# Optimization experiments

Hardware: AMD Instinct MI355X
Metric: run time of the kernel (lower is better)

The kernel has to match this reference:

```python
import jax, jax.numpy as jnp
import numpy as np

N_NODES = 100000
N_EDGES = 1600000
IN_C, HID_C, OUT_C = 256, 128, 256


def setup_inputs() -> dict:
    key = jax.random.key(0)
    ks = jax.random.split(key, 8)
    x = jax.random.normal(ks[0], (N_NODES, IN_C), dtype=jnp.float32)
    src = jax.random.randint(ks[1], (N_EDGES,), 0, N_NODES, dtype=jnp.int64)
    dst = jnp.sort(jax.random.randint(ks[2], (N_EDGES,), 0, N_NODES, dtype=jnp.int64))
    # GraphConv weight [in, hid] (glorot), bias [hid]
    W_conv = jax.random.normal(ks[3], (IN_C, HID_C), dtype=jnp.float32) * (2.0 / (IN_C + HID_C)) ** 0.5
    b_conv = jnp.zeros((HID_C,), dtype=jnp.float32)
    # torch Linear weights are [out, in]
    W1 = jax.random.normal(ks[4], (HID_C, HID_C), dtype=jnp.float32) * (2.0 / (2 * HID_C)) ** 0.5
    b1 = jax.random.uniform(ks[5], (HID_C,), dtype=jnp.float32, minval=-1.0, maxval=1.0) / np.sqrt(HID_C)
    W2 = jax.random.normal(ks[6], (OUT_C, HID_C), dtype=jnp.float32) * (2.0 / (HID_C + OUT_C)) ** 0.5
    b2 = jax.random.uniform(ks[7], (OUT_C,), dtype=jnp.float32, minval=-1.0, maxval=1.0) / np.sqrt(OUT_C)
    return {"x": x, "src": src, "dst": dst, "W_conv": W_conv, "b_conv": b_conv,
            "W1": W1, "b1": b1, "W2": W2, "b2": b2}


def reference(x, src, dst, W_conv, b_conv, W1, b1, W2, b2):
    N = x.shape[0]
    ones = jnp.ones(src.shape[0], dtype=x.dtype)
    out_deg = jnp.clip(jax.ops.segment_sum(ones, src, num_segments=N), 1.0)  # [N]
    in_deg = jnp.clip(jax.ops.segment_sum(ones, dst, num_segments=N), 1.0)   # [N]
    # DGL GraphConv, norm='both', in_feats > out_feats -> weight applied before aggregation
    h = x * jax.lax.rsqrt(out_deg)[:, None]          # src-side normalization
    h = h @ W_conv                                    # [N, hid]
    m = jax.ops.segment_sum(h[src], dst, num_segments=N, indices_are_sorted=True)
    h = m * jax.lax.rsqrt(in_deg)[:, None] + b_conv   # dst-side normalization + bias
    h = jax.nn.relu(h)
    h = jax.nn.relu(h @ W1.T + b1)
    return h @ W2.T + b2
```

## Files before the change

### kernel.cpp

```cpp
#include <hip/hip_runtime.h>
#include <hip/hip_bf16.h>


typedef __attribute__((ext_vector_type(8))) short short8;
typedef __attribute__((ext_vector_type(4))) float f32x4;

static __device__ __forceinline__ float bf2f(unsigned int u16) {
    union { unsigned int i; float f; } c; c.i = u16 << 16; return c.f;
}
static __device__ __forceinline__ ushort f2bf(float f) {
    union { float f; unsigned int i; } c; c.f = f;
    unsigned int i = c.i;
    return (ushort)((i + 0x7FFFu + ((i >> 16) & 1u)) >> 16);
}

constexpr int NCHUNK   = 256;
constexpr int NBUK_MAX = 512;

__global__ __launch_bounds__(256) void hist1_kernel(
    const int* __restrict__ src, int* __restrict__ M, int nE, int nBuk, int chunkSz)
{
    __shared__ int cnt[NBUK_MAX];
    int c = blockIdx.x, tid = threadIdx.x;
    for (int i = tid; i < nBuk; i += 256) cnt[i] = 0;
    __syncthreads();
    int e0 = c * chunkSz, e1 = min(e0 + chunkSz, nE);
    for (int e = e0 + tid; e < e1; e += 256)
        atomicAdd(&cnt[src[e] >> 8], 1);
    __syncthreads();
    for (int b = tid; b < nBuk; b += 256)
        M[b * NCHUNK + c] = cnt[b];
}

__global__ __launch_bounds__(256) void scanA_kernel(
    int* __restrict__ M, int* __restrict__ tot)
{
    __shared__ int buf[2][NCHUNK];
    int b = blockIdx.x, tid = threadIdx.x;
    int v = M[b * NCHUNK + tid];
    buf[0][tid] = v;
    __syncthreads();
    int pi = 0;
#pragma unroll
    for (int off = 1; off < NCHUNK; off <<= 1) {
        int t = buf[pi][tid];
        if (tid >= off) t += buf[pi][tid - off];
        buf[pi ^ 1][tid] = t;
        __syncthreads();
        pi ^= 1;
    }
    int incl = buf[pi][tid];
    M[b * NCHUNK + tid] = incl - v;
    if (tid == NCHUNK - 1) tot[b] = incl;
}

__global__ __launch_bounds__(512) void scanB_kernel(
    const int* __restrict__ tot, int* __restrict__ bucket_base, int nBuk)
{
    __shared__ int t_l[NBUK_MAX], base_l[NBUK_MAX + 1];
    int tid = threadIdx.x;
    if (tid < nBuk) t_l[tid] = tot[tid];
    __syncthreads();
    if (tid == 0) {
        int base = 0;
        for (int i = 0; i < nBuk; ++i) { base_l[i] = base; base += t_l[i]; }
        base_l[nBuk] = base;
    }
    __syncthreads();
    if (tid <= nBuk) bucket_base[tid] = base_l[tid];
}

__global__ __launch_bounds__(256) void scatter_keys_kernel(
    const int* __restrict__ src, const int* __restrict__ M,
    const int* __restrict__ bucket_base, int* __restrict__ ss,
    int nE, int nBuk, int chunkSz)
{
    __shared__ int cur[NBUK_MAX];
    int c = blockIdx.x, tid = threadIdx.x;
    for (int i = tid; i < nBuk; i += 256)
        cur[i] = M[i * NCHUNK + c] + bucket_base[i];
    __syncthreads();
    int e0 = c * chunkSz, e1 = min(e0 + chunkSz, nE);
    for (int e = e0 + tid; e < e1; e += 256) {
        int s = src[e];
        int pos = atomicAdd(&cur[s >> 8], 1);
        ss[pos] = s;
    }
}

__global__ __launch_bounds__(256) void count_kernel(
    const int* __restrict__ ss, const int* __restrict__ bucket_base,
    int* __restrict__ outdeg, int N)
{
    __shared__ int hist[256];
    int b = blockIdx.x, tid = threadIdx.x;
    hist[tid] = 0;
    __syncthreads();
    int e0 = bucket_base[b], e1 = bucket_base[b + 1];
    for (int e = e0 + tid; e < e1; e += 256)
        atomicAdd(&hist[ss[e] & 255], 1);
    __syncthreads();
    int n = b * 256 + tid;
    if (n < N) outdeg[n] = hist[tid];
}

__global__ __launch_bounds__(256) void rowptr_kernel(
    const int* __restrict__ dst, int* __restrict__ row_ptr, int nE, int N)
{
    int e = blockIdx.x * 256 + threadIdx.x;
    if (e >= nE) return;
    int d = dst[e];
    if (e == 0) {
        for (int n = 0; n <= d; ++n) row_ptr[n] = 0;
    } else {
        int p = dst[e - 1];
        for (int n = p + 1; n <= d; ++n) row_ptr[n] = e;
    }
    if (e == nE - 1) {
        for (int n = d + 1; n <= N; ++n) row_ptr[n] = nE;
    }
}

__global__ __launch_bounds__(256) void wprep_kernel(
    const float* __restrict__ Wc, const float* __restrict__ W1,
    const float* __restrict__ W2, ushort* __restrict__ WcT,
    ushort* __restrict__ W1b, ushort* __restrict__ W2b)
{
    int i = blockIdx.x * 256 + threadIdx.x;
    if (i < 128 * 256) {
        int o = i >> 8, k = i & 255;
        WcT[o * 256 + k] = f2bf(Wc[k * 128 + o]);
    } else if (i < 128 * 256 + 128 * 128) {
        int j = i - 128 * 256;
        W1b[j] = f2bf(W1[j]);
    } else if (i < 128 * 256 + 128 * 128 + 256 * 128) {
        int j = i - 128 * 256 - 128 * 128;
        W2b[j] = f2bf(W2[j]);
    }
}

__global__ __launch_bounds__(512, 4) void gemm1_kernel(
    const float* __restrict__ A, const ushort* __restrict__ B,
    ushort* __restrict__ C, int nRows)
{
    __shared__ ushort Bs[128 * 256];
    __shared__ ushort As[128 * 64];

    const int tid  = threadIdx.x;
    const int lane = tid & 63;
    const int w    = tid >> 6;
    const int wm   = w >> 1;
    const int wn   = w & 1;
    const int r    = lane & 15;
    const int q    = lane >> 4;
    const int row0 = blockIdx.x * 128;

#pragma unroll
    for (int s = 0; s < 8; ++s) {
        int idx = s * 512 + tid;
        int col = idx >> 5, kg = idx & 31;
        *(short8*)&Bs[col * 256 + ((kg ^ (col & 7)) * 8)] =
            *(const short8*)&B[(size_t)col * 256 + kg * 8];
    }

    int arow0 = tid >> 3,          akg0 = tid & 7;
    int arow1 = (512 + tid) >> 3,  akg1 = (512 + tid) & 7;

    float4 areg[2][2][2];

#define G1_ISSUE(cc, bb)                                                     \
    {                                                                        \
        int g0 = row0 + arow0, g1 = row0 + arow1;                            \
        areg[bb][0][0] = make_float4(0.f, 0.f, 0.f, 0.f);                    \
        areg[bb][0][1] = make_float4(0.f, 0.f, 0.f, 0.f);                    \
        areg[bb][1][0] = make_float4(0.f, 0.f, 0.f, 0.f);                    \
        areg[bb][1][1] = make_float4(0.f, 0.f, 0.f, 0.f);                    \
        if (g0 < nRows) {                                                    \
            const float* p = &A[(size_t)g0 * 256 + (cc) * 64 + akg0 * 8];    \
            areg[bb][0][0] = *(const float4*)p;                              \
            areg[bb][0][1] = *(const float4*)(p + 4);                        \
        }                                                                    \
        if (g1 < nRows) {                                                    \
            const float* p = &A[(size_t)g1 * 256 + (cc) * 64 + akg1 * 8];    \
            areg[bb][1][0] = *(const float4*)p;                              \
            areg[bb][1][1] = *(const float4*)(p + 4);                        \
        }                                                                    \
    }

    G1_ISSUE(0, 0)
    G1_ISSUE(1, 1)

    f32x4 acc[8];
#pragma unroll
    for (int t = 0; t < 8; ++t) acc[t] = (f32x4){0.f, 0.f, 0.f, 0.f};

#pragma unroll
    for (int c = 0; c < 4; ++c) {
        if (c > 0) __syncthreads();
        const int buf = c & 1;
#pragma unroll
        for (int s = 0; s < 2; ++s) {
            int arow = s ? arow1 : arow0;
            int akg  = s ? akg1  : akg0;
            float4 v0 = areg[buf][s][0], v1 = areg[buf][s][1];
            ushort u[8];
            u[0] = f2bf(v0.x); u[1] = f2bf(v0.y); u[2] = f2bf(v0.z); u[3] = f2bf(v0.w);
            u[4] = f2bf(v1.x); u[5] = f2bf(v1.y); u[6] = f2bf(v1.z); u[7] = f2bf(v1.w);
            *(short8*)&As[arow * 64 + ((akg ^ (arow & 7)) * 8)] = *(const short8*)u;
        }
        if (c + 2 < 4) G1_ISSUE(c + 2, buf)
        __syncthreads();
#pragma unroll
        for (int ks = 0; ks < 2; ++ks) {
            int sA = ks * 4 + q;
            int ra0 = wm * 32 + r, ra1 = wm * 32 + 16 + r;
            short8 a0 = *(const short8*)&As[ra0 * 64 + ((sA ^ (ra0 & 7)) * 8)];
            short8 a1 = *(const short8*)&As[ra1 * 64 + ((sA ^ (ra1 & 7)) * 8)];
            int sB = c * 8 + ks * 4 + q;
#pragma unroll
            for (int t = 0; t < 4; ++t) {
                int col = wn * 64 + t * 16 + r;
                short8 b = *(const short8*)&Bs[col * 256 + ((sB ^ (col & 7)) * 8)];
                acc[t]     = __builtin_amdgcn_mfma_f32_16x16x32_bf16(a0, b, acc[t], 0, 0, 0);
                acc[4 + t] = __builtin_amdgcn_mfma_f32_16x16x32_bf16(a1, b, acc[4 + t], 0, 0, 0);
            }
        }
    }
#undef G1_ISSUE

#pragma unroll
    for (int fr = 0; fr < 2; ++fr)
#pragma unroll
        for (int t = 0; t < 4; ++t) {
            int col = wn * 64 + t * 16 + r;
#pragma unroll
            for (int reg = 0; reg < 4; ++reg) {
                int g = row0 + wm * 32 + fr * 16 + q * 4 + reg;
                if (g < nRows)
                    C[(size_t)g * 128 + col] = f2bf(acc[fr * 4 + t][reg]);
            }
        }
}

__global__ __launch_bounds__(256) void gather_kernel(
    const ushort* __restrict__ h1, const int* __restrict__ src,
    const int* __restrict__ rp, const int* __restrict__ outdeg,
    const float* __restrict__ b_conv, ushort* __restrict__ h2, int N)
{
    int n = (blockIdx.x * 256 + threadIdx.x) >> 6;
    int lane = threadIdx.x & 63;
    if (n >= N) return;
    const int g = lane >> 4;
    const int c = lane & 15;
    int e0 = rp[n], e1 = rp[n + 1];

    float a[8];
#pragma unroll
    for (int j = 0; j < 8; ++j) a[j] = 0.f;

    int e = e0 + g;
    for (; e + 4 < e1; e += 8) {
        int s0 = src[e], s1 = src[e + 4];
        float sc0 = rsqrtf((float)max(outdeg[s0], 1));
        float sc1 = rsqrtf((float)max(outdeg[s1], 1));
        short8 v0 = *(const short8*)&h1[(size_t)s0 * 128 + c * 8];
        short8 v1 = *(const short8*)&h1[(size_t)s1 * 128 + c * 8];
#pragma unroll
        for (int j = 0; j < 8; ++j)
            a[j] = fmaf(sc0, bf2f((unsigned short)v0[j]),
                        fmaf(sc1, bf2f((unsigned short)v1[j]), a[j]));
    }
    if (e < e1) {
        int s0 = src[e];
        float sc0 = rsqrtf((float)max(outdeg[s0], 1));
        short8 v0 = *(const short8*)&h1[(size_t)s0 * 128 + c * 8];
#pragma unroll
        for (int j = 0; j < 8; ++j)
            a[j] = fmaf(sc0, bf2f((unsigned short)v0[j]), a[j]);
    }

#pragma unroll
    for (int j = 0; j < 8; ++j) {
        a[j] += __shfl_xor(a[j], 16, 64);
        a[j] += __shfl_xor(a[j], 32, 64);
    }

    if (g == 0) {
        float sc = rsqrtf((float)max(e1 - e0, 1));
        ushort o[8];
#pragma unroll
        for (int j = 0; j < 8; ++j)
            o[j] = f2bf(fmaxf(fmaf(a[j], sc, b_conv[c * 8 + j]), 0.f));
        *(short8*)&h2[(size_t)n * 128 + c * 8] = *(const short8*)o;
    }
}

__global__ __launch_bounds__(512, 2) void gemm23_kernel(
    const ushort* __restrict__ A, const ushort* __restrict__ W1b,
    const ushort* __restrict__ W2b, const float* __restrict__ b1,
    const float* __restrict__ b2, float* __restrict__ out, int nRows)
{
    __shared__ ushort AsTs[128 * 128];
    __shared__ ushort W1s[128 * 128];
    __shared__ ushort W2s[256 * 128];

    const int tid  = threadIdx.x;
    const int lane = tid & 63;
    const int w    = tid >> 6;
    const int wm   = w >> 1;
    const int wn   = w & 1;
    const int r    = lane & 15;
    const int q    = lane >> 4;
    const int row0 = blockIdx.x * 128;

#pragma unroll
    for (int s = 0; s < 4; ++s) {
        int idx = s * 512 + tid;
        int row = idx >> 4, kg = idx & 15;
        int g = row0 + row;
        short8 v = (short8){0, 0, 0, 0, 0, 0, 0, 0};
        if (g < nRows) v = *(const short8*)&A[(size_t)g * 128 + kg * 8];
        *(short8*)&AsTs[row * 128 + ((kg ^ (row & 7)) * 8)] = v;
    }
#pragma unroll
    for (int s = 0; s < 4; ++s) {
        int idx = s * 512 + tid;
        int col = idx >> 4, kg = idx & 15;
        *(short8*)&W1s[col * 128 + ((kg ^ (col & 7)) * 8)] =
            *(const short8*)&W1b[(size_t)col * 128 + kg * 8];
    }
#pragma unroll
    for (int s = 0; s < 8; ++s) {
        int idx = s * 512 + tid;
        int col = idx >> 4, kg = idx & 15;
        *(short8*)&W2s[col * 128 + ((kg ^ (col & 7)) * 8)] =
            *(const short8*)&W2b[(size_t)col * 128 + kg * 8];
    }
    __syncthreads();

    f32x4 acc1[8];
#pragma unroll
    for (int t = 0; t < 8; ++t) acc1[t] = (f32x4){0.f, 0.f, 0.f, 0.f};
#pragma unroll
    for (int ks = 0; ks < 4; ++ks) {
        int sA = ks * 4 + q;
        int ra0 = wm * 32 + r, ra1 = wm * 32 + 16 + r;
        short8 a0 = *(const short8*)&AsTs[ra0 * 128 + ((sA ^ (ra0 & 7)) * 8)];
        short8 a1 = *(const short8*)&AsTs[ra1 * 128 + ((sA ^ (ra1 & 7)) * 8)];
#pragma unroll
        for (int t = 0; t < 4; ++t) {
            int col = wn * 64 + t * 16 + r;
            short8 b = *(const short8*)&W1s[col * 128 + ((sA ^ (col & 7)) * 8)];
            acc1[t]     = __builtin_amdgcn_mfma_f32_16x16x32_bf16(a0, b, acc1[t], 0, 0, 0);
            acc1[4 + t] = __builtin_amdgcn_mfma_f32_16x16x32_bf16(a1, b, acc1[4 + t], 0, 0, 0);
        }
    }
    __syncthreads();

#pragma unroll
    for (int fr = 0; fr < 2; ++fr)
#pragma unroll
        for (int t = 0; t < 4; ++t) {
            int col = wn * 64 + t * 16 + r;
            float bo = b1[col];
#pragma unroll
            for (int reg = 0; reg < 4; ++reg) {
                int row = wm * 32 + fr * 16 + q * 4 + reg;
                float v = fmaxf(acc1[fr * 4 + t][reg] + bo, 0.f);
                AsTs[row * 128 + (((col >> 3) ^ (row & 7)) * 8) + (col & 7)] = f2bf(v);
            }
        }
    __syncthreads();

    f32x4 acc2[16];
#pragma unroll
    for (int t = 0; t < 16; ++t) acc2[t] = (f32x4){0.f, 0.f, 0.f, 0.f};
#pragma unroll
    for (int ks = 0; ks < 4; ++ks) {
        int sA = ks * 4 + q;
        int ra0 = wm * 32 + r, ra1 = wm * 32 + 16 + r;
        short8 a0 = *(const short8*)&AsTs[ra0 * 128 + ((sA ^ (ra0 & 7)) * 8)];
        short8 a1 = *(const short8*)&AsTs[ra1 * 128 + ((sA ^ (ra1 & 7)) * 8)];
#pragma unroll
        for (int t = 0; t < 8; ++t) {
            int col = wn * 128 + t * 16 + r;
            short8 b = *(const short8*)&W2s[col * 128 + ((sA ^ (col & 7)) * 8)];
            acc2[t]     = __builtin_amdgcn_mfma_f32_16x16x32_bf16(a0, b, acc2[t], 0, 0, 0);
            acc2[8 + t] = __builtin_amdgcn_mfma_f32_16x16x32_bf16(a1, b, acc2[8 + t], 0, 0, 0);
        }
    }

#pragma unroll
    for (int fr = 0; fr < 2; ++fr)
#pragma unroll
        for (int t = 0; t < 8; ++t) {
            int col = wn * 128 + t * 16 + r;
            float bo = b2[col];
#pragma unroll
            for (int reg = 0; reg < 4; ++reg) {
                int g = row0 + wm * 32 + fr * 16 + q * 4 + reg;
                if (g < nRows)
                    out[(size_t)g * 256 + col] = acc2[fr * 8 + t][reg] + bo;
            }
        }
}

extern "C" void kernel_launch(void* const* d_in, const int* in_sizes, int n_in,
                              void* d_out, int out_size, void* d_ws, size_t ws_size,
                              hipStream_t stream)
{
    const float* x      = (const float*)d_in[0];
    const int*   src    = (const int*)d_in[1];
    const int*   dst    = (const int*)d_in[2];
    const float* W_conv = (const float*)d_in[3];
    const float* b_conv = (const float*)d_in[4];
    const float* W1     = (const float*)d_in[5];
    const float* b1     = (const float*)d_in[6];
    const float* W2     = (const float*)d_in[7];
    const float* b2     = (const float*)d_in[8];
    float* out = (float*)d_out;

    const int N  = in_sizes[0] / 256;
    const int nE = in_sizes[1];

    const int nBuk    = (N + 255) >> 8;
    const int chunkSz = (nE + NCHUNK - 1) / NCHUNK;

    ushort* h1  = (ushort*)d_ws;
    ushort* h2  = h1 + (size_t)N * 128;
    ushort* WcT = h2 + (size_t)N * 128;
    ushort* W1b = WcT + 128 * 256;
    ushort* W2b = W1b + 128 * 128;
    int* outdeg = (int*)(W2b + 256 * 128);
    int* rp     = outdeg + N;
    int* bb     = rp + (N + 1);
    int* tot    = bb + (nBuk + 1);
    int* M      = tot + nBuk;
    int* ss     = M + nBuk * NCHUNK;

    wprep_kernel<<<(128 * 256 + 128 * 128 + 256 * 128 + 255) / 256, 256, 0, stream>>>(
        W_conv, W1, W2, WcT, W1b, W2b);

    hist1_kernel<<<NCHUNK, 256, 0, stream>>>(src, M, nE, nBuk, chunkSz);
    scanA_kernel<<<nBuk, 256, 0, stream>>>(M, tot);
    scanB_kernel<<<1, 512, 0, stream>>>(tot, bb, nBuk);
    scatter_keys_kernel<<<NCHUNK, 256, 0, stream>>>(src, M, bb, ss, nE, nBuk, chunkSz);
    count_kernel<<<nBuk, 256, 0, stream>>>(ss, bb, outdeg, N);

    const int nBlocks128 = (N + 127) / 128;
    gemm1_kernel<<<nBlocks128, 512, 0, stream>>>(x, WcT, h1, N);

    rowptr_kernel<<<(nE + 255) / 256, 256, 0, stream>>>(dst, rp, nE, N);

    gather_kernel<<<(N * 64 + 255) / 256, 256, 0, stream>>>(
        h1, src, rp, outdeg, b_conv, h2, N);

    gemm23_kernel<<<nBlocks128, 512, 0, stream>>>(h2, W1b, W2b, b1, b2, out, N);
}
```

Measured before the change: 185.4 us.

## Merge prep kernels, fold out-degree scaling into GEMM1, unroll gather by four

Weight conversion, the source histogram and the row-pointer build now run as separate block ranges of one prep kernel, removing two launches. The src-side rsqrt(out_deg) scale is applied per row in the GEMM1 epilogue, using the algebraic equivalence of scaling before or after the matmul, rather than per edge in the gather. The gather no longer does random outdeg lookups or rsqrt per edge, and processes four edges per iteration to raise memory-level parallelism. The trade-off is a slightly different rounding order, since the scale is applied before bf16 rounding.

```diff
diff --git a/kernel.cpp b/kernel.cpp
--- a/kernel.cpp
+++ b/kernel.cpp
@@ -16,98 +16,46 @@
 
 constexpr int NCHUNK   = 256;
 constexpr int NBUK_MAX = 512;
-
-__global__ __launch_bounds__(256) void hist1_kernel(
-    const int* __restrict__ src, int* __restrict__ M, int nE, int nBuk, int chunkSz)
+constexpr int WPREP_BLOCKS = (128 * 256 + 128 * 128 + 256 * 128) / 256;
+
+__global__ __launch_bounds__(256) void prep_kernel(
+    const float* __restrict__ Wc, const float* __restrict__ W1,
+    const float* __restrict__ W2, ushort* __restrict__ WcT,
+    ushort* __restrict__ W1b, ushort* __restrict__ W2b,
+    const int* __restrict__ src, int* __restrict__ M,
+    const int* __restrict__ dst, int* __restrict__ row_ptr,
+    int nE, int N, int nBuk, int chunkSz)
 {
     __shared__ int cnt[NBUK_MAX];
-    int c = blockIdx.x, tid = threadIdx.x;
-    for (int i = tid; i < nBuk; i += 256) cnt[i] = 0;
-    __syncthreads();
-    int e0 = c * chunkSz, e1 = min(e0 + chunkSz, nE);
-    for (int e = e0 + tid; e < e1; e += 256)
-        atomicAdd(&cnt[src[e] >> 8], 1);
-    __syncthreads();
-    for (int b = tid; b < nBuk; b += 256)
-        M[b * NCHUNK + c] = cnt[b];
-}
-
-__global__ __launch_bounds__(256) void scanA_kernel(
-    int* __restrict__ M, int* __restrict__ tot)
-{
-    __shared__ int buf[2][NCHUNK];
-    int b = blockIdx.x, tid = threadIdx.x;
-    int v = M[b * NCHUNK + tid];
-    buf[0][tid] = v;
-    __syncthreads();
-    int pi = 0;
-#pragma unroll
-    for (int off = 1; off < NCHUNK; off <<= 1) {
-        int t = buf[pi][tid];
-        if (tid >= off) t += buf[pi][tid - off];
-        buf[pi ^ 1][tid] = t;
+    const int bid = blockIdx.x, tid = threadIdx.x;
+
+    if (bid < WPREP_BLOCKS) {
+        int i = bid * 256 + tid;
+        if (i < 128 * 256) {
+            int o = i >> 8, k = i & 255;
+            WcT[o * 256 + k] = f2bf(Wc[k * 128 + o]);
+        } else if (i < 128 * 256 + 128 * 128) {
+            int j = i - 128 * 256;
+            W1b[j] = f2bf(W1[j]);
+        } else {
+            int j = i - 128 * 256 - 128 * 128;
+            W2b[j] = f2bf(W2[j]);
+        }
+        return;
+    }
+    if (bid < WPREP_BLOCKS + NCHUNK) {
+        int c = bid - WPREP_BLOCKS;
+        for (int i = tid; i < nBuk; i += 256) cnt[i] = 0;
         __syncthreads();
-        pi ^= 1;
-    }
-    int incl = buf[pi][tid];
-    M[b * NCHUNK + tid] = incl - v;
-    if (tid == NCHUNK - 1) tot[b] = incl;
-}
-
-__global__ __launch_bounds__(512) void scanB_kernel(
-    const int* __restrict__ tot, int* __restrict__ bucket_base, int nBuk)
-{
-    __shared__ int t_l[NBUK_MAX], base_l[NBUK_MAX + 1];
-    int tid = threadIdx.x;
-    if (tid < nBuk) t_l[tid] = tot[tid];
-    __syncthreads();
-    if (tid == 0) {
-        int base = 0;
-        for (int i = 0; i < nBuk; ++i) { base_l[i] = base; base += t_l[i]; }
-        base_l[nBuk] = base;
-    }
-    __syncthreads();
-    if (tid <= nBuk) bucket_base[tid] = base_l[tid];
-}
-
-__global__ __launch_bounds__(256) void scatter_keys_kernel(
-    const int* __restrict__ src, const int* __restrict__ M,
-    const int* __restrict__ bucket_base, int* __restrict__ ss,
-    int nE, int nBuk, int chunkSz)
-{
-    __shared__ int cur[NBUK_MAX];
-    int c = blockIdx.x, tid = threadIdx.x;
-    for (int i = tid; i < nBuk; i += 256)
-        cur[i] = M[i * NCHUNK + c] + bucket_base[i];
-    __syncthreads();
-    int e0 = c * chunkSz, e1 = min(e0 + chunkSz, nE);
-    for (int e = e0 + tid; e < e1; e += 256) {
-        int s = src[e];
-        int pos = atomicAdd(&cur[s >> 8], 1);
-        ss[pos] = s;
-    }
-}
-
-__global__ __launch_bounds__(256) void count_kernel(
-    const int* __restrict__ ss, const int* __restrict__ bucket_base,
-    int* __restrict__ outdeg, int N)
-{
-    __shared__ int hist[256];
-    int b = blockIdx.x, tid = threadIdx.x;
-    hist[tid] = 0;
-    __syncthreads();
-    int e0 = bucket_base[b], e1 = bucket_base[b + 1];
-    for (int e = e0 + tid; e < e1; e += 256)
-        atomicAdd(&hist[ss[e] & 255], 1);
-    __syncthreads();
-    int n = b * 256 + tid;
-    if (n < N) outdeg[n] = hist[tid];
-}
-
-__global__ __launch_bounds__(256) void rowptr_kernel(
-    const int* __restrict__ dst, int* __restrict__ row_ptr, int nE, int N)
-{
-    int e = blockIdx.x * 256 + threadIdx.x;
+        int e0 = c * chunkSz, e1 = min(e0 + chunkSz, nE);
+        for (int e = e0 + tid; e < e1; e += 256)
+            atomicAdd(&cnt[src[e] >> 8], 1);
+        __syncthreads();
+        for (int b = tid; b < nBuk; b += 256)
+            M[b * NCHUNK + c] = cnt[b];
+        return;
+    }
+    int e = (bid - WPREP_BLOCKS - NCHUNK) * 256 + tid;
     if (e >= nE) return;
     int d = dst[e];
     if (e == 0) {
@@ -121,30 +69,85 @@
     }
 }
 
-__global__ __launch_bounds__(256) void wprep_kernel(
-    const float* __restrict__ Wc, const float* __restrict__ W1,
-    const float* __restrict__ W2, ushort* __restrict__ WcT,
-    ushort* __restrict__ W1b, ushort* __restrict__ W2b)
-{
-    int i = blockIdx.x * 256 + threadIdx.x;
-    if (i < 128 * 256) {
-        int o = i >> 8, k = i & 255;
-        WcT[o * 256 + k] = f2bf(Wc[k * 128 + o]);
-    } else if (i < 128 * 256 + 128 * 128) {
-        int j = i - 128 * 256;
-        W1b[j] = f2bf(W1[j]);
-    } else if (i < 128 * 256 + 128 * 128 + 256 * 128) {
-        int j = i - 128 * 256 - 128 * 128;
-        W2b[j] = f2bf(W2[j]);
-    }
+__global__ __launch_bounds__(256) void scanA_kernel(
+    int* __restrict__ M, int* __restrict__ tot)
+{
+    __shared__ int buf[2][NCHUNK];
+    int b = blockIdx.x, tid = threadIdx.x;
+    int v = M[b * NCHUNK + tid];
+    buf[0][tid] = v;
+    __syncthreads();
+    int pi = 0;
+#pragma unroll
+    for (int off = 1; off < NCHUNK; off <<= 1) {
+        int t = buf[pi][tid];
+        if (tid >= off) t += buf[pi][tid - off];
+        buf[pi ^ 1][tid] = t;
+        __syncthreads();
+        pi ^= 1;
+    }
+    int incl = buf[pi][tid];
+    M[b * NCHUNK + tid] = incl - v;
+    if (tid == NCHUNK - 1) tot[b] = incl;
+}
+
+__global__ __launch_bounds__(512) void scanB_kernel(
+    const int* __restrict__ tot, int* __restrict__ bucket_base, int nBuk)
+{
+    __shared__ int t_l[NBUK_MAX], base_l[NBUK_MAX + 1];
+    int tid = threadIdx.x;
+    if (tid < nBuk) t_l[tid] = tot[tid];
+    __syncthreads();
+    if (tid == 0) {
+        int base = 0;
+        for (int i = 0; i < nBuk; ++i) { base_l[i] = base; base += t_l[i]; }
+        base_l[nBuk] = base;
+    }
+    __syncthreads();
+    if (tid <= nBuk) bucket_base[tid] = base_l[tid];
+}
+
+__global__ __launch_bounds__(256) void scatter_keys_kernel(
+    const int* __restrict__ src, const int* __restrict__ M,
+    const int* __restrict__ bucket_base, int* __restrict__ ss,
+    int nE, int nBuk, int chunkSz)
+{
+    __shared__ int cur[NBUK_MAX];
+    int c = blockIdx.x, tid = threadIdx.x;
+    for (int i = tid; i < nBuk; i += 256)
+        cur[i] = M[i * NCHUNK + c] + bucket_base[i];
+    __syncthreads();
+    int e0 = c * chunkSz, e1 = min(e0 + chunkSz, nE);
+    for (int e = e0 + tid; e < e1; e += 256) {
+        int s = src[e];
+        int pos = atomicAdd(&cur[s >> 8], 1);
+        ss[pos] = s;
+    }
+}
+
+__global__ __launch_bounds__(256) void count_kernel(
+    const int* __restrict__ ss, const int* __restrict__ bucket_base,
+    int* __restrict__ outdeg, int N)
+{
+    __shared__ int hist[256];
+    int b = blockIdx.x, tid = threadIdx.x;
+    hist[tid] = 0;
+    __syncthreads();
+    int e0 = bucket_base[b], e1 = bucket_base[b + 1];
+    for (int e = e0 + tid; e < e1; e += 256)
+        atomicAdd(&hist[ss[e] & 255], 1);
+    __syncthreads();
+    int n = b * 256 + tid;
+    if (n < N) outdeg[n] = hist[tid];
 }
 
 __global__ __launch_bounds__(512, 4) void gemm1_kernel(
     const float* __restrict__ A, const ushort* __restrict__ B,
-    ushort* __restrict__ C, int nRows)
+    const int* __restrict__ outdeg, ushort* __restrict__ C, int nRows)
 {
     __shared__ ushort Bs[128 * 256];
     __shared__ ushort As[128 * 64];
+    __shared__ float rowscale[128];
 
     const int tid  = threadIdx.x;
     const int lane = tid & 63;
@@ -154,6 +157,12 @@
     const int r    = lane & 15;
     const int q    = lane >> 4;
     const int row0 = blockIdx.x * 128;
+
+    if (tid < 128) {
+        int g = row0 + tid;
+        int dv = (g < nRows) ? outdeg[g] : 1;
+        rowscale[tid] = rsqrtf((float)max(dv, 1));
+    }
 
 #pragma unroll
     for (int s = 0; s < 8; ++s) {
@@ -235,17 +244,18 @@
             int col = wn * 64 + t * 16 + r;
 #pragma unroll
             for (int reg = 0; reg < 4; ++reg) {
-                int g = row0 + wm * 32 + fr * 16 + q * 4 + reg;
+                int lr = wm * 32 + fr * 16 + q * 4 + reg;
+                int g = row0 + lr;
                 if (g < nRows)
-                    C[(size_t)g * 128 + col] = f2bf(acc[fr * 4 + t][reg]);
+                    C[(size_t)g * 128 + col] = f2bf(acc[fr * 4 + t][reg] * rowscale[lr]);
             }
         }
 }
 
 __global__ __launch_bounds__(256) void gather_kernel(
     const ushort* __restrict__ h1, const int* __restrict__ src,
-    const int* __restrict__ rp, const int* __restrict__ outdeg,
-    const float* __restrict__ b_conv, ushort* __restrict__ h2, int N)
+    const int* __restrict__ rp, const float* __restrict__ b_conv,
+    ushort* __restrict__ h2, int N)
 {
     int n = (blockIdx.x * 256 + threadIdx.x) >> 6;
     int lane = threadIdx.x & 63;
@@ -259,24 +269,22 @@
     for (int j = 0; j < 8; ++j) a[j] = 0.f;
 
     int e = e0 + g;
-    for (; e + 4 < e1; e += 8) {
-        int s0 = src[e], s1 = src[e + 4];
-        float sc0 = rsqrtf((float)max(outdeg[s0], 1));
-        float sc1 = rsqrtf((float)max(outdeg[s1], 1));
-        short8 v0 = *(const short8*)&h1[(size_t)s0 * 128 + c * 8];
-        short8 v1 = *(const short8*)&h1[(size_t)s1 * 128 + c * 8];
+    for (; e + 12 < e1; e += 16) {
+        int s0 = src[e], s1 = src[e + 4], s2 = src[e + 8], s3 = src[e + 12];
+        short8 v0 = *(const short8*)&h1[((size_t)(unsigned)s0 << 7) + c * 8];
+        short8 v1 = *(const short8*)&h1[((size_t)(unsigned)s1 << 7) + c * 8];
+        short8 v2 = *(const short8*)&h1[((size_t)(unsigned)s2 << 7) + c * 8];
+        short8 v3 = *(const short8*)&h1[((size_t)(unsigned)s3 << 7) + c * 8];
 #pragma unroll
         for (int j = 0; j < 8; ++j)
-            a[j] = fmaf(sc0, bf2f((unsigned short)v0[j]),
-                        fmaf(sc1, bf2f((unsigned short)v1[j]), a[j]));
-    }
-    if (e < e1) {
-        int s0 = src[e];
-        float sc0 = rsqrtf((float)max(outdeg[s0], 1));
-        short8 v0 = *(const short8*)&h1[(size_t)s0 * 128 + c * 8];
+            a[j] += (bf2f((unsigned short)v0[j]) + bf2f((unsigned short)v1[j]))
+                  + (bf2f((unsigned short)v2[j]) + bf2f((unsigned short)v3[j]));
+    }
+    for (; e < e1; e += 4) {
+        short8 v0 = *(const short8*)&h1[((size_t)(unsigned)src[e] << 7) + c * 8];
 #pragma unroll
         for (int j = 0; j < 8; ++j)
-            a[j] = fmaf(sc0, bf2f((unsigned short)v0[j]), a[j]);
+            a[j] += bf2f((unsigned short)v0[j]);
     }
 
 #pragma unroll
@@ -291,7 +299,7 @@
 #pragma unroll
         for (int j = 0; j < 8; ++j)
             o[j] = f2bf(fmaxf(fmaf(a[j], sc, b_conv[c * 8 + j]), 0.f));
-        *(short8*)&h2[(size_t)n * 128 + c * 8] = *(const short8*)o;
+        *(short8*)&h2[((size_t)(unsigned)n << 7) + c * 8] = *(const short8*)o;
     }
 }
 
@@ -438,22 +446,20 @@
     int* M      = tot + nBuk;
     int* ss     = M + nBuk * NCHUNK;
 
-    wprep_kernel<<<(128 * 256 + 128 * 128 + 256 * 128 + 255) / 256, 256, 0, stream>>>(
-        W_conv, W1, W2, WcT, W1b, W2b);
-
-    hist1_kernel<<<NCHUNK, 256, 0, stream>>>(src, M, nE, nBuk, chunkSz);
+    const int rowptrBlocks = (nE + 255) / 256;
+    prep_kernel<<<WPREP_BLOCKS + NCHUNK + rowptrBlocks, 256, 0, stream>>>(
+        W_conv, W1, W2, WcT, W1b, W2b, src, M, dst, rp, nE, N, nBuk, chunkSz);
+
     scanA_kernel<<<nBuk, 256, 0, stream>>>(M, tot);
     scanB_kernel<<<1, 512, 0, stream>>>(tot, bb, nBuk);
     scatter_keys_kernel<<<NCHUNK, 256, 0, stream>>>(src, M, bb, ss, nE, nBuk, chunkSz);
     count_kernel<<<nBuk, 256, 0, stream>>>(ss, bb, outdeg, N);
 
     const int nBlocks128 = (N + 127) / 128;
-    gemm1_kernel<<<nBlocks128, 512, 0, stream>>>(x, WcT, h1, N);
-
-    rowptr_kernel<<<(nE + 255) / 256, 256, 0, stream>>>(dst, rp, nE, N);
+    gemm1_kernel<<<nBlocks128, 512, 0, stream>>>(x, WcT, outdeg, h1, N);
 
     gather_kernel<<<(N * 64 + 255) / 256, 256, 0, stream>>>(
-        h1, src, rp, outdeg, b_conv, h2, N);
+        h1, src, rp, b_conv, h2, N);
 
     gemm23_kernel<<<nBlocks128, 512, 0, stream>>>(h2, W1b, W2b, b1, b2, out, N);
 }
```

After: 184.8 us. About the same (-0.3%).
